# Kernel tuning notes

Measured on AMD Instinct MI355X. Metric: run time of the kernel, lower is better.

Reference implementation:

```python
import jax, jax.numpy as jnp
import numpy as np

DIM = 96
HEADS = 8
HH = 128
WW = 128
L = HH * WW
K = 256
B = 2


def setup_inputs() -> dict:
    key = jax.random.key(0)
    ks = jax.random.split(key, 8)
    s = 0.02
    return {
        "x": jax.random.normal(ks[0], (B, L, DIM), jnp.float32),
        "Wqkv": jax.random.normal(ks[1], (DIM, 3 * DIM), jnp.float32) * s,
        "W0": jax.random.normal(ks[2], (DIM, DIM), jnp.float32) * s,
        "E": jax.random.normal(ks[3], (L, K), jnp.float32) * s,
        "conv0_w": jax.random.normal(ks[4], (DIM, 1, 5, 5), jnp.float32) * s,
        "conv0_b": jnp.zeros((DIM,), jnp.float32),
        "conv_sp_w": jax.random.normal(ks[5], (DIM, 1, 7, 7), jnp.float32) * s,
        "conv_sp_b": jnp.zeros((DIM,), jnp.float32),
        "conv1_w": jax.random.normal(ks[6], (DIM, DIM, 1, 1), jnp.float32) * s,
        "conv1_b": jnp.zeros((DIM,), jnp.float32),
        "H": HH,
        "W": WW,
    }


def _conv(x, w, b, pad, dil, groups):
    y = jax.lax.conv_general_dilated(
        x, w, window_strides=(1, 1), padding=[(pad, pad), (pad, pad)],
        rhs_dilation=(dil, dil),
        dimension_numbers=("NCHW", "OIHW", "NCHW"),
        feature_group_count=groups)
    return y + b[None, :, None, None]


def _cnn_atten(x, H, W, conv0_w, conv0_b, conv_sp_w, conv_sp_b, conv1_w, conv1_b):
    # VAN-style Large-Kernel-Attention: dw5x5 -> dw7x7(dil=3) -> 1x1, gate by identity
    Bx, Lx, C = x.shape
    xi = x.reshape(Bx, H, W, C).transpose(0, 3, 1, 2)  # B,C,H,W
    a = _conv(xi, conv0_w, conv0_b, 2, 1, C)
    a = _conv(a, conv_sp_w, conv_sp_b, 9, 3, C)
    a = _conv(a, conv1_w, conv1_b, 0, 1, 1)
    out = xi * a
    return out.transpose(0, 2, 3, 1).reshape(Bx, Lx, C)


def reference(x, Wqkv, W0, E, conv0_w, conv0_b, conv_sp_w, conv_sp_b, conv1_w, conv1_b, H, W):
    Bx, Lx, C = x.shape
    dh = C // HEADS
    scale = dh ** (-0.5)
    qkv = (x @ Wqkv).reshape(Bx, Lx, 3, HEADS, dh).transpose(2, 0, 3, 1, 4)  # 3,B,h,L,d
    q, k, v = qkv[0], qkv[1], qkv[2]
    ca = _cnn_atten(x, H, W, conv0_w, conv0_b, conv_sp_w, conv_sp_b, conv1_w, conv1_b)  # B,L,C
    vf = v.transpose(0, 2, 1, 3).reshape(Bx, Lx, C)
    vf = ca * vf  # elementwise CNN gating of V
    v = vf.reshape(Bx, Lx, HEADS, dh).transpose(0, 2, 1, 3)  # B,h,L,d
    # Linformer-style sequence reduction: L -> K
    v = jnp.einsum("bhjd,jk->bhkd", v, E)
    k = jnp.einsum("bhjd,jk->bhkd", k, E)
    attn = jax.nn.softmax(jnp.einsum("bhid,bhkd->bhik", q, k) * scale, axis=-1)  # B,h,L,K
    o = jnp.einsum("bhik,bhkd->bhid", attn, v)
    o = o.transpose(0, 2, 1, 3).reshape(Bx, Lx, C)
    return o @ W0
```

## Files before the change

kernel.cpp:

```cpp
#include <hip/hip_runtime.h>

#define HH_ 128
#define WW_ 128
#define LL_ (HH_*WW_)
#define NH 8
#define DHD 12
#define KD 256
#define BB_ 2
#define NROW (BB_*LL_)

typedef __attribute__((ext_vector_type(8))) short short8v;
typedef __attribute__((ext_vector_type(4))) float f32x4;
typedef unsigned short ushortT;

__device__ __forceinline__ float4 ld4(const float* p) {
    return *reinterpret_cast<const float4*>(p);
}
__device__ __forceinline__ unsigned int pk2(float a, float b) {
    unsigned int ua = __float_as_uint(a);
    unsigned int ub = __float_as_uint(b);
    ua = (ua + 0x7FFFu + ((ua >> 16) & 1u)) >> 16;
    ub = (ub + 0x7FFFu + ((ub >> 16) & 1u)) >> 16;
    return ua | (ub << 16);
}
__device__ __forceinline__ ushortT bf1(float a) {
    unsigned int u = __float_as_uint(a);
    return (ushortT)((u + 0x7FFFu + ((u >> 16) & 1u)) >> 16);
}
__device__ __forceinline__ float ubf(ushortT v) {
    return __uint_as_float(((unsigned int)v) << 16);
}
__device__ __forceinline__ unsigned int cvtpk(float a, float b) {
    unsigned int r;
    asm("v_cvt_pk_bf16_f32 %0, %1, %2" : "=v"(r) : "v"(a), "v"(b));
    return r;
}

__global__ __launch_bounds__(256) void k_prep(const float* __restrict__ E,
        const float* __restrict__ Wq, const float* __restrict__ W0,
        const float* __restrict__ w1, ushortT* __restrict__ ET,
        ushortT* __restrict__ wqT, ushortT* __restrict__ w0T,
        ushortT* __restrict__ w1c) {
    __shared__ ushortT Tz[64*66];
    const int tid = threadIdx.x;
    if (blockIdx.x < 1024) {
        const int jt = blockIdx.x >> 2, kt = blockIdx.x & 3;
        const int j0 = jt * 64, kk0 = kt * 64;
        for (int i = tid; i < 64*16; i += 256) {
            int row = i >> 4, s4 = (i & 15) << 2;
            float4 e4 = ld4(&E[(long)(j0 + row)*256 + kk0 + s4]);
            Tz[(s4 + 0)*66 + row] = bf1(e4.x);
            Tz[(s4 + 1)*66 + row] = bf1(e4.y);
            Tz[(s4 + 2)*66 + row] = bf1(e4.z);
            Tz[(s4 + 3)*66 + row] = bf1(e4.w);
        }
        __syncthreads();
        unsigned int* Tu = (unsigned int*)Tz;
        for (int i = tid; i < 64*32; i += 256) {
            int kk = i >> 5, s = i & 31;
            ((unsigned int*)ET)[(((long)(kk0 + kk) << 14) + j0 >> 1) + s] = Tu[kk*33 + s];
        }
    } else {
        int i = (blockIdx.x - 1024)*256 + tid;
        if (i < 27648) {
            int n = i / 96, k = i % 96;
            wqT[n*96 + k] = bf1(Wq[k*288 + n]);
        } else if (i < 36864) {
            int j = i - 27648;
            int n = j / 96, k = j % 96;
            w0T[n*96 + k] = bf1(W0[k*96 + n]);
        } else if (i < 46080) {
            int j = i - 36864;
            w1c[j] = bf1(w1[j]);
        }
    }
}

__global__ __launch_bounds__(256) void k_qkv(const float* __restrict__ x,
        const ushortT* __restrict__ wqT, ushortT* __restrict__ qkv16) {
    __shared__ ushortT xb[64*104];
    const int tid = threadIdx.x;
    const int r0w = blockIdx.x * 64;
    for (int i = tid; i < 64*48; i += 256) {
        int r = i / 48, cp = i % 48;
        const float* sp = x + (long)(r0w + r)*96 + cp*2;
        ((unsigned int*)xb)[r*52 + cp] = pk2(sp[0], sp[1]);
    }
    __syncthreads();
    const int lane = tid & 63, wv = tid >> 6;
    const int l15 = lane & 15, l4 = lane >> 4;
    short8v bx[3];
#pragma unroll
    for (int kt = 0; kt < 3; ++kt)
        bx[kt] = *(const short8v*)((const short*)xb + (wv*16 + l15)*104 + kt*32 + l4*8);
#pragma unroll 2
    for (int mt = 0; mt < 18; ++mt) {
        f32x4 acc = {0.f, 0.f, 0.f, 0.f};
#pragma unroll
        for (int kt = 0; kt < 3; ++kt) {
            short8v a = *(const short8v*)((const short*)wqT + (mt*16 + l15)*96 + kt*32 + l4*8);
            acc = __builtin_amdgcn_mfma_f32_16x16x32_bf16(a, bx[kt], acc, 0, 0, 0);
        }
        unsigned int* q32 = (unsigned int*)(qkv16 + (long)(r0w + wv*16 + l15)*288 + mt*16 + l4*4);
        q32[0] = pk2(acc[0], acc[1]);
        q32[1] = pk2(acc[2], acc[3]);
    }
}

__global__ __launch_bounds__(256) void k_dw5(const float* __restrict__ xin,
                                             const float* __restrict__ w,
                                             const float* __restrict__ bias,
                                             float* __restrict__ out) {
    __shared__ float wl[25][96];
    const int tid = threadIdx.x;
    for (int i = tid; i < 25*96; i += 256) {
        int c = i / 25, t = i % 25;
        wl[t][c] = w[i];
    }
    __syncthreads();
    const int c4 = (tid & 7)*4;
    const int px = tid >> 3;
    const int pix0 = blockIdx.x * 32;
    const int b = pix0 >> 14;
    const int y = (pix0 & 16383) >> 7;
    const int xx = (pix0 & 127) + px;
    float4 acc[3];
#pragma unroll
    for (int ch = 0; ch < 3; ++ch) { acc[ch].x=0.f; acc[ch].y=0.f; acc[ch].z=0.f; acc[ch].w=0.f; }
#pragma unroll
    for (int iy = 0; iy < 5; ++iy) {
        int y2 = y + iy - 2;
        if (y2 < 0 || y2 >= HH_) continue;
#pragma unroll
        for (int ix = 0; ix < 5; ++ix) {
            int x2 = xx + ix - 2;
            if (x2 < 0 || x2 >= WW_) continue;
            const float* src = xin + ((b << 14) + y2*WW_ + x2)*96;
            const float* wt = &wl[iy*5 + ix][0];
#pragma unroll
            for (int ch = 0; ch < 3; ++ch) {
                float4 xv = ld4(src + ch*32 + c4);
                float4 wv = ld4(wt + ch*32 + c4);
                acc[ch].x = fmaf(xv.x, wv.x, acc[ch].x);
                acc[ch].y = fmaf(xv.y, wv.y, acc[ch].y);
                acc[ch].z = fmaf(xv.z, wv.z, acc[ch].z);
                acc[ch].w = fmaf(xv.w, wv.w, acc[ch].w);
            }
        }
    }
    float* dst = out + (long)(pix0 + px)*96;
#pragma unroll
    for (int ch = 0; ch < 3; ++ch) {
        float4 bv = ld4(bias + ch*32 + c4);
        float4 r;
        r.x = acc[ch].x + bv.x; r.y = acc[ch].y + bv.y;
        r.z = acc[ch].z + bv.z; r.w = acc[ch].w + bv.w;
        *reinterpret_cast<float4*>(dst + ch*32 + c4) = r;
    }
}

__global__ __launch_bounds__(256) void k_dw7(const float* __restrict__ xin,
                                             const float* __restrict__ w,
                                             const float* __restrict__ bias,
                                             float* __restrict__ out) {
    __shared__ float wl[49][96];
    const int tid = threadIdx.x;
    for (int i = tid; i < 49*96; i += 256) {
        int c = i / 49, t = i % 49;
        wl[t][c] = w[i];
    }
    __syncthreads();
    const int c4 = (tid & 7)*4;
    const int px = tid >> 3;
    const int pix0 = blockIdx.x * 32;
    const int b = pix0 >> 14;
    const int y = (pix0 & 16383) >> 7;
    const int xx = (pix0 & 127) + px;
    float4 acc[3];
#pragma unroll
    for (int ch = 0; ch < 3; ++ch) { acc[ch].x=0.f; acc[ch].y=0.f; acc[ch].z=0.f; acc[ch].w=0.f; }
#pragma unroll
    for (int iy = 0; iy < 7; ++iy) {
        int y2 = y + iy*3 - 9;
        if (y2 < 0 || y2 >= HH_) continue;
#pragma unroll
        for (int ix = 0; ix < 7; ++ix) {
            int x2 = xx + ix*3 - 9;
            if (x2 < 0 || x2 >= WW_) continue;
            const float* src = xin + ((b << 14) + y2*WW_ + x2)*96;
            const float* wt = &wl[iy*7 + ix][0];
#pragma unroll
            for (int ch = 0; ch < 3; ++ch) {
                float4 xv = ld4(src + ch*32 + c4);
                float4 wv = ld4(wt + ch*32 + c4);
                acc[ch].x = fmaf(xv.x, wv.x, acc[ch].x);
                acc[ch].y = fmaf(xv.y, wv.y, acc[ch].y);
                acc[ch].z = fmaf(xv.z, wv.z, acc[ch].z);
                acc[ch].w = fmaf(xv.w, wv.w, acc[ch].w);
            }
        }
    }
    float* dst = out + (long)(pix0 + px)*96;
#pragma unroll
    for (int ch = 0; ch < 3; ++ch) {
        float4 bv = ld4(bias + ch*32 + c4);
        float4 r;
        r.x = acc[ch].x + bv.x; r.y = acc[ch].y + bv.y;
        r.z = acc[ch].z + bv.z; r.w = acc[ch].w + bv.w;
        *reinterpret_cast<float4*>(dst + ch*32 + c4) = r;
    }
}

__global__ __launch_bounds__(256) void k_pw_gate(const float* __restrict__ a2,
        const ushortT* __restrict__ w1c, const float* __restrict__ b1,
        const float* __restrict__ xin, const ushortT* __restrict__ qkv16,
        ushortT* __restrict__ XT) {
    __shared__ ushortT ab[64*104];
    __shared__ ushortT ktile[96*66];
    __shared__ ushortT vtile[96*66];
    const int tid = threadIdx.x;
    const int r0 = blockIdx.x * 64;
    const int b = r0 >> 14, j0 = r0 & 16383;
    for (int i = tid; i < 64*48; i += 256) {
        int r = i / 48, cp = i % 48;
        const float* sp = a2 + (long)(r0 + r)*96 + cp*2;
        ((unsigned int*)ab)[r*52 + cp] = pk2(sp[0], sp[1]);
    }
    const unsigned int* q32 = (const unsigned int*)qkv16;
    for (int i = tid; i < 64*48; i += 256) {
        int row = i / 48, cp = i % 48;
        unsigned int kk2 = q32[(long)(r0 + row)*144 + 48 + cp];
        ktile[(2*cp + 0)*66 + row] = (ushortT)(kk2 & 0xFFFF);
        ktile[(2*cp + 1)*66 + row] = (ushortT)(kk2 >> 16);
    }
    __syncthreads();
    const int lane = tid & 63, wv = tid >> 6;
    const int l15 = lane & 15, l4 = lane >> 4;
    const int row = r0 + wv*16 + l15;
    const int jloc = wv*16 + l15;
    short8v bx[3];
#pragma unroll
    for (int kt = 0; kt < 3; ++kt)
        bx[kt] = *(const short8v*)((const short*)ab + (wv*16 + l15)*104 + kt*32 + l4*8);
#pragma unroll
    for (int mt = 0; mt < 6; ++mt) {
        f32x4 acc = {0.f, 0.f, 0.f, 0.f};
#pragma unroll
        for (int kt = 0; kt < 3; ++kt) {
            short8v a = *(const short8v*)((const short*)w1c + (mt*16 + l15)*96 + kt*32 + l4*8);
            acc = __builtin_amdgcn_mfma_f32_16x16x32_bf16(a, bx[kt], acc, 0, 0, 0);
        }
        const int c0 = mt*16 + l4*4;
        float4 b4 = ld4(&b1[c0]);
        float4 x4 = ld4(&xin[(long)row*96 + c0]);
        uint2 vv = *reinterpret_cast<const uint2*>(qkv16 + (long)row*288 + 192 + c0);
        float v0 = ubf((ushortT)(vv.x & 0xFFFF)), v1 = ubf((ushortT)(vv.x >> 16));
        float v2 = ubf((ushortT)(vv.y & 0xFFFF)), v3 = ubf((ushortT)(vv.y >> 16));
        vtile[(c0 + 0)*66 + jloc] = bf1(x4.x * v0 * (acc[0] + b4.x));
        vtile[(c0 + 1)*66 + jloc] = bf1(x4.y * v1 * (acc[1] + b4.y));
        vtile[(c0 + 2)*66 + jloc] = bf1(x4.z * v2 * (acc[2] + b4.z));
        vtile[(c0 + 3)*66 + jloc] = bf1(x4.w * v3 * (acc[3] + b4.w));
    }
    __syncthreads();
    unsigned int* XTu = (unsigned int*)XT;
    unsigned int* ku = (unsigned int*)ktile;
    unsigned int* vu = (unsigned int*)vtile;
    for (int i = tid; i < 96*32; i += 256) {
        int cc = i >> 5, s = i & 31;
        XTu[((((long)b*192 + cc) << 14) + j0 >> 1) + s] = ku[cc*33 + s];
    }
    for (int i = tid; i < 96*32; i += 256) {
        int cc = i >> 5, s = i & 31;
        XTu[((((long)b*192 + 96 + cc) << 14) + j0 >> 1) + s] = vu[cc*33 + s];
    }
}

__global__ __launch_bounds__(512, 2) void k_ered(const ushortT* __restrict__ ET,
        const ushortT* __restrict__ XT, ushortT* __restrict__ part16) {
    const int tid = threadIdx.x;
    const int lane = tid & 63, wv = tid >> 6;
    const int l15 = lane & 15, l4 = lane >> 4;
    const int mtg = wv & 3, nth = wv >> 2;
    const int b  = blockIdx.x >> 7;
    const int jc = blockIdx.x & 127;
    const int j0 = jc * 128;
    f32x4 acc[4][6];
#pragma unroll
    for (int mi = 0; mi < 4; ++mi)
#pragma unroll
        for (int ni = 0; ni < 6; ++ni)
            acc[mi][ni] = (f32x4){0.f, 0.f, 0.f, 0.f};
    const ushortT* Ab = ET + ((long)(mtg*64 + l15) << 14) + j0 + l4*8;
    const ushortT* Bb = XT + (((long)b*192 + nth*96 + l15) << 14) + j0 + l4*8;
#pragma unroll
    for (int ks = 0; ks < 4; ++ks) {
        short8v a[4], bx[6];
#pragma unroll
        for (int mi = 0; mi < 4; ++mi)
            a[mi] = *(const short8v*)(Ab + ((long)mi << 18) + ks*32);
#pragma unroll
        for (int ni = 0; ni < 6; ++ni)
            bx[ni] = *(const short8v*)(Bb + ((long)ni << 18) + ks*32);
#pragma unroll
        for (int mi = 0; mi < 4; ++mi)
#pragma unroll
            for (int ni = 0; ni < 6; ++ni)
                acc[mi][ni] = __builtin_amdgcn_mfma_f32_16x16x32_bf16(a[mi], bx[ni], acc[mi][ni], 0, 0, 0);
    }
    const long base = (long)(b*128 + jc)*49152;
#pragma unroll
    for (int mi = 0; mi < 4; ++mi) {
        int kkb = (mtg*4 + mi)*16 + l4*4;
#pragma unroll
        for (int ni = 0; ni < 6; ++ni) {
            int cc = (nth*6 + ni)*16 + l15;
#pragma unroll
            for (int r = 0; r < 4; ++r)
                part16[base + (long)(kkb + r)*192 + cc] = bf1(acc[mi][ni][r]);
        }
    }
}

__global__ __launch_bounds__(256) void k_ered_fin(const ushortT* __restrict__ part16,
        ushortT* __restrict__ kp16, ushortT* __restrict__ vp16) {
    const int idx = blockIdx.x*256 + threadIdx.x;
    const int c  = idx % 96;
    const int kk = (idx / 96) % 256;
    const int m  = (idx / (96*256)) % 2;
    const int b  = idx / (96*256*2);
    float s = 0.f;
    long off = ((long)(b*128)*256 + kk)*192 + m*96 + c;
    for (int jc = 0; jc < 128; ++jc) {
        s += ubf(part16[off]);
        off += 49152;
    }
    const int h = c / DHD, d = c % DHD;
    if (m == 0) {
        kp16[((b*NH + h)*256 + kk)*16 + d] = bf1(s * 0.4164701998f);
        if (d < 4) kp16[((b*NH + h)*256 + kk)*16 + 12 + d] = 0;
    } else {
        vp16[((b*NH + h)*16 + d)*256 + kk] = bf1(s);
        if (d < 4)
            vp16[((b*NH + h)*16 + 12 + d)*256 + kk] = (d == 0) ? (ushortT)0x3F80 : (ushortT)0;
    }
}

__global__ __launch_bounds__(256, 4) void k_attn(const ushortT* __restrict__ qkv16,
        const ushortT* __restrict__ kp16, const ushortT* __restrict__ vp16,
        ushortT* __restrict__ obuf) {
    __shared__ ushortT Pl[4][4096];
    const int tid = threadIdx.x;
    const int lane = tid & 63, wv = tid >> 6;
    const int l15 = lane & 15, l4 = lane >> 4;
    const int bid = blockIdx.x;
    const int r0 = (bid >> 1) * 32;
    const int hgrp = bid & 1;
    const int b = r0 >> 14;
    ushortT* Pw = &Pl[wv][0];
    unsigned int* Pu = (unsigned int*)Pw;
    const int wbase = (l4 >> 1)*64 + l15*4 + (l4 & 1)*2;
    const f32x4 z = {0.f, 0.f, 0.f, 0.f};
    const int h = wv + hgrp*4;
    const ushortT* kpb = kp16 + ((long)(b*NH + h) << 12) + l15*16 + l4*8;
    const ushortT* vb  = vp16 + (((long)(b*NH + h)*16 + l15) << 8) + l4*8;
    short8v a[16];
#pragma unroll
    for (int mt = 0; mt < 16; ++mt)
        a[mt] = *(const short8v*)(kpb + mt*256);
#pragma unroll
    for (int nt = 0; nt < 2; ++nt) {
        short8v bq = {0, 0, 0, 0, 0, 0, 0, 0};
        {
            unsigned int* bq32 = (unsigned int*)&bq;
            const ushortT* qp = qkv16 + (long)(r0 + nt*16 + l15)*288 + h*12;
            if (l4 == 0) {
                uint2 t0 = *reinterpret_cast<const uint2*>(qp);
                uint2 t1 = *reinterpret_cast<const uint2*>(qp + 4);
                bq32[0] = t0.x; bq32[1] = t0.y; bq32[2] = t1.x; bq32[3] = t1.y;
            } else if (l4 == 1) {
                uint2 t0 = *reinterpret_cast<const uint2*>(qp + 8);
                bq32[0] = t0.x; bq32[1] = t0.y;
            }
        }
#pragma unroll
        for (int mt = 0; mt < 16; ++mt) {
            f32x4 s = __builtin_amdgcn_mfma_f32_16x16x32_bf16(a[mt], bq, z, 0, 0, 0);
            unsigned int* dst = Pu + (mt >> 1)*256 + (mt & 1)*128 + wbase;
            dst[0] = cvtpk(exp2f(s[0]), exp2f(s[1]));
            dst[1] = cvtpk(exp2f(s[2]), exp2f(s[3]));
        }
        f32x4 o = z;
#pragma unroll
        for (int ks = 0; ks < 8; ++ks) {
            short8v bp = *(const short8v*)(Pw + ks*512 + l4*128 + l15*8);
            short8v av = *(const short8v*)(vb + ks*32);
            o = __builtin_amdgcn_mfma_f32_16x16x32_bf16(av, bp, o, 0, 0, 0);
        }
        float rinv = 1.0f / __shfl(o[0], 48 + l15, 64);
        if (l4 < 3) {
            unsigned int* od = (unsigned int*)(obuf + (long)(r0 + nt*16 + l15)*96 + h*12 + l4*4);
            od[0] = cvtpk(o[0]*rinv, o[1]*rinv);
            od[1] = cvtpk(o[2]*rinv, o[3]*rinv);
        }
    }
}

__global__ __launch_bounds__(256) void k_out(const ushortT* __restrict__ obuf,
        const ushortT* __restrict__ w0T, float* __restrict__ out) {
    __shared__ ushortT ol[64*104];
    const int tid = threadIdx.x;
    const int r0 = blockIdx.x * 64;
    for (int i = tid; i < 768; i += 256) {
        int r = i / 12, sg = i % 12;
        *reinterpret_cast<uint4*>(&ol[r*104 + sg*8]) =
            *reinterpret_cast<const uint4*>(&obuf[(long)(r0 + r)*96 + sg*8]);
    }
    __syncthreads();
    const int lane = tid & 63, wv = tid >> 6;
    const int l15 = lane & 15, l4 = lane >> 4;
    short8v a[3];
#pragma unroll
    for (int kt = 0; kt < 3; ++kt)
        a[kt] = *(const short8v*)((const short*)ol + (wv*16 + l15)*104 + kt*32 + l4*8);
#pragma unroll
    for (int nt = 0; nt < 6; ++nt) {
        f32x4 acc = {0.f, 0.f, 0.f, 0.f};
#pragma unroll
        for (int kt = 0; kt < 3; ++kt) {
            short8v bw = *(const short8v*)((const short*)w0T + (nt*16 + l15)*96 + kt*32 + l4*8);
            acc = __builtin_amdgcn_mfma_f32_16x16x32_bf16(a[kt], bw, acc, 0, 0, 0);
        }
#pragma unroll
        for (int r = 0; r < 4; ++r)
            out[(long)(r0 + wv*16 + l4*4 + r)*96 + nt*16 + l15] = acc[r];
    }
}

extern "C" void kernel_launch(void* const* d_in, const int* in_sizes, int n_in,
                              void* d_out, int out_size, void* d_ws, size_t ws_size,
                              hipStream_t stream) {
    (void)in_sizes; (void)n_in; (void)out_size; (void)ws_size;
    const float* x    = (const float*)d_in[0];
    const float* Wqkv = (const float*)d_in[1];
    const float* W0   = (const float*)d_in[2];
    const float* E    = (const float*)d_in[3];
    const float* c0w  = (const float*)d_in[4];
    const float* c0b  = (const float*)d_in[5];
    const float* cspw = (const float*)d_in[6];
    const float* cspb = (const float*)d_in[7];
    const float* c1w  = (const float*)d_in[8];
    const float* c1b  = (const float*)d_in[9];
    float* out = (float*)d_out;
    float* ws  = (float*)d_ws;

    ushortT* qkv16  = (ushortT*)ws;
    ushortT* wqT16  = (ushortT*)(ws + 4718592);
    ushortT* w0T16  = (ushortT*)(ws + 4732416);
    ushortT* w1c16  = (ushortT*)(ws + 4737024);
    ushortT* ET16   = (ushortT*)(ws + 4741632);
    ushortT* XT16   = (ushortT*)(ws + 6838784);
    float* a1   = ws + 9984512;
    float* a2   = ws + 13130240;
    ushortT* part16 = (ushortT*)(ws + 9984512);
    ushortT* obuf   = (ushortT*)(ws + 9984512);
    ushortT* kp16   = (ushortT*)(ws + 16275968);
    ushortT* vp16   = (ushortT*)(ws + 16308736);

    k_prep<<<dim3(1204), dim3(256), 0, stream>>>(E, Wqkv, W0, c1w, ET16, wqT16, w0T16, w1c16);
    k_qkv<<<dim3(NROW/64), dim3(256), 0, stream>>>(x, wqT16, qkv16);
    k_dw5<<<dim3(NROW/32), dim3(256), 0, stream>>>(x, c0w, c0b, a1);
    k_dw7<<<dim3(NROW/32), dim3(256), 0, stream>>>(a1, cspw, cspb, a2);
    k_pw_gate<<<dim3(NROW/64), dim3(256), 0, stream>>>(a2, w1c16, c1b, x, qkv16, XT16);
    k_ered<<<dim3(256), dim3(512), 0, stream>>>(ET16, XT16, part16);
    k_ered_fin<<<dim3(384), dim3(256), 0, stream>>>(part16, kp16, vp16);
    k_attn<<<dim3(NROW/16), dim3(256), 0, stream>>>(qkv16, kp16, vp16, obuf);
    k_out<<<dim3(NROW/64), dim3(256), 0, stream>>>(obuf, w0T16, out);
}
```

Baseline: 147.3 us.

## Stage per-head K/V projections in LDS and remap attention blocks to one head

Each attention block now handles a single head over 64 rows (one 16-row tile per wave) rather than four heads over 32 rows. The block cooperatively loads that head's reduced K and V tiles into shared memory, with V padded to avoid bank conflicts, and waves read their MFMA operands from there. This drops the per-wave register-resident K fragments and the redundant global K/V loads across waves. In exchange it adds a block barrier, uses more LDS per block (about 49 KB), and each wave does only one row tile, so less work is spread over the fixed load cost.

```diff
diff --git a/kernel.cpp b/kernel.cpp
--- a/kernel.cpp
+++ b/kernel.cpp
@@ -348,60 +348,69 @@
 __global__ __launch_bounds__(256, 4) void k_attn(const ushortT* __restrict__ qkv16,
         const ushortT* __restrict__ kp16, const ushortT* __restrict__ vp16,
         ushortT* __restrict__ obuf) {
-    __shared__ ushortT Pl[4][4096];
+    __shared__ ushortT lds[24720];
     const int tid = threadIdx.x;
     const int lane = tid & 63, wv = tid >> 6;
     const int l15 = lane & 15, l4 = lane >> 4;
     const int bid = blockIdx.x;
-    const int r0 = (bid >> 1) * 32;
-    const int hgrp = bid & 1;
+    const int r0 = (bid >> 3) * 64;
+    const int h = bid & 7;
     const int b = r0 >> 14;
-    ushortT* Pw = &Pl[wv][0];
+    {
+        const uint4* ksrc = (const uint4*)(kp16 + ((long)(b*NH + h) << 12));
+        uint4* kdst = (uint4*)lds;
+        kdst[tid] = ksrc[tid];
+        kdst[256 + tid] = ksrc[256 + tid];
+        const uint4* vsrc = (const uint4*)(vp16 + ((long)(b*NH + h) << 12));
+        uint4* vdst = (uint4*)(lds + 4112);
+        int r1 = tid >> 5, s1 = tid & 31;
+        vdst[r1*33 + s1] = vsrc[tid];
+        int j2 = tid + 256;
+        int r2 = j2 >> 5, s2 = j2 & 31;
+        vdst[r2*33 + s2] = vsrc[j2];
+        if (tid < 2) ((uint4*)(lds + 4096))[tid] = (uint4){0u, 0u, 0u, 0u};
+    }
+    __syncthreads();
+    ushortT* Pw = lds + 8336 + wv*4096;
     unsigned int* Pu = (unsigned int*)Pw;
     const int wbase = (l4 >> 1)*64 + l15*4 + (l4 & 1)*2;
     const f32x4 z = {0.f, 0.f, 0.f, 0.f};
-    const int h = wv + hgrp*4;
-    const ushortT* kpb = kp16 + ((long)(b*NH + h) << 12) + l15*16 + l4*8;
-    const ushortT* vb  = vp16 + (((long)(b*NH + h)*16 + l15) << 8) + l4*8;
-    short8v a[16];
-#pragma unroll
-    for (int mt = 0; mt < 16; ++mt)
-        a[mt] = *(const short8v*)(kpb + mt*256);
-#pragma unroll
-    for (int nt = 0; nt < 2; ++nt) {
-        short8v bq = {0, 0, 0, 0, 0, 0, 0, 0};
-        {
-            unsigned int* bq32 = (unsigned int*)&bq;
-            const ushortT* qp = qkv16 + (long)(r0 + nt*16 + l15)*288 + h*12;
-            if (l4 == 0) {
-                uint2 t0 = *reinterpret_cast<const uint2*>(qp);
-                uint2 t1 = *reinterpret_cast<const uint2*>(qp + 4);
-                bq32[0] = t0.x; bq32[1] = t0.y; bq32[2] = t1.x; bq32[3] = t1.y;
-            } else if (l4 == 1) {
-                uint2 t0 = *reinterpret_cast<const uint2*>(qp + 8);
-                bq32[0] = t0.x; bq32[1] = t0.y;
-            }
-        }
-#pragma unroll
-        for (int mt = 0; mt < 16; ++mt) {
-            f32x4 s = __builtin_amdgcn_mfma_f32_16x16x32_bf16(a[mt], bq, z, 0, 0, 0);
-            unsigned int* dst = Pu + (mt >> 1)*256 + (mt & 1)*128 + wbase;
-            dst[0] = cvtpk(exp2f(s[0]), exp2f(s[1]));
-            dst[1] = cvtpk(exp2f(s[2]), exp2f(s[3]));
-        }
-        f32x4 o = z;
-#pragma unroll
-        for (int ks = 0; ks < 8; ++ks) {
-            short8v bp = *(const short8v*)(Pw + ks*512 + l4*128 + l15*8);
-            short8v av = *(const short8v*)(vb + ks*32);
-            o = __builtin_amdgcn_mfma_f32_16x16x32_bf16(av, bp, o, 0, 0, 0);
-        }
-        float rinv = 1.0f / __shfl(o[0], 48 + l15, 64);
-        if (l4 < 3) {
-            unsigned int* od = (unsigned int*)(obuf + (long)(r0 + nt*16 + l15)*96 + h*12 + l4*4);
-            od[0] = cvtpk(o[0]*rinv, o[1]*rinv);
-            od[1] = cvtpk(o[2]*rinv, o[3]*rinv);
-        }
+    const int row0 = r0 + wv*16;
+    short8v bq = {0, 0, 0, 0, 0, 0, 0, 0};
+    {
+        unsigned int* bq32 = (unsigned int*)&bq;
+        const ushortT* qp = qkv16 + (long)(row0 + l15)*288 + h*12;
+        if (l4 == 0) {
+            uint2 t0 = *reinterpret_cast<const uint2*>(qp);
+            uint2 t1 = *reinterpret_cast<const uint2*>(qp + 4);
+            bq32[0] = t0.x; bq32[1] = t0.y; bq32[2] = t1.x; bq32[3] = t1.y;
+        } else if (l4 == 1) {
+            uint2 t0 = *reinterpret_cast<const uint2*>(qp + 8);
+            bq32[0] = t0.x; bq32[1] = t0.y;
+        }
+    }
+    const ushortT* kpl = lds + l15*16 + l4*8;
+#pragma unroll
+    for (int mt = 0; mt < 16; ++mt) {
+        short8v a = *(const short8v*)(kpl + mt*256);
+        f32x4 s = __builtin_amdgcn_mfma_f32_16x16x32_bf16(a, bq, z, 0, 0, 0);
+        unsigned int* dst = Pu + (mt >> 1)*256 + (mt & 1)*128 + wbase;
+        dst[0] = cvtpk(exp2f(s[0]), exp2f(s[1]));
+        dst[1] = cvtpk(exp2f(s[2]), exp2f(s[3]));
+    }
+    f32x4 o = z;
+    const ushortT* vpl = lds + 4112 + l15*264 + l4*8;
+#pragma unroll
+    for (int ks = 0; ks < 8; ++ks) {
+        short8v bp = *(const short8v*)(Pw + ks*512 + l4*128 + l15*8);
+        short8v av = *(const short8v*)(vpl + ks*32);
+        o = __builtin_amdgcn_mfma_f32_16x16x32_bf16(av, bp, o, 0, 0, 0);
+    }
+    float rinv = 1.0f / __shfl(o[0], 48 + l15, 64);
+    if (l4 < 3) {
+        unsigned int* od = (unsigned int*)(obuf + (long)(row0 + l15)*96 + h*12 + l4*4);
+        od[0] = cvtpk(o[0]*rinv, o[1]*rinv);
+        od[1] = cvtpk(o[2]*rinv, o[3]*rinv);
     }
 }
 
@@ -473,6 +482,6 @@
     k_pw_gate<<<dim3(NROW/64), dim3(256), 0, stream>>>(a2, w1c16, c1b, x, qkv16, XT16);
     k_ered<<<dim3(256), dim3(512), 0, stream>>>(ET16, XT16, part16);
     k_ered_fin<<<dim3(384), dim3(256), 0, stream>>>(part16, kp16, vp16);
-    k_attn<<<dim3(NROW/16), dim3(256), 0, stream>>>(qkv16, kp16, vp16, obuf);
+    k_attn<<<dim3((NROW/64)*NH), dim3(256), 0, stream>>>(qkv16, kp16, vp16, obuf);
     k_out<<<dim3(NROW/64), dim3(256), 0, stream>>>(obuf, w0T16, out);
 }
```

New measurement: 145.6 us. No clear change (-1.2%).
